# Performance work log

Hardware: AMD Instinct MI355X
Metric: run time of the kernel (lower is better)

The kernel has to match this reference:

```python
import jax, jax.numpy as jnp
import numpy as np

HIDDEN = 1024
N_HEADS = 16
HEAD_DIM = HIDDEN // N_HEADS  # 64


def setup_inputs() -> dict:
    key = jax.random.key(0)
    ks = jax.random.split(key, 5)
    B, S = 4, 4096
    x = jax.random.normal(ks[0], (B, S, HIDDEN), dtype=jnp.float32)
    scale = 1.0 / np.sqrt(HIDDEN)
    wq = jax.random.normal(ks[1], (HIDDEN, HIDDEN), dtype=jnp.float32) * scale
    wk = jax.random.normal(ks[2], (HIDDEN, HIDDEN), dtype=jnp.float32) * scale
    wv = jax.random.normal(ks[3], (HIDDEN, HIDDEN), dtype=jnp.float32) * scale
    wo = jax.random.normal(ks[4], (HIDDEN, HIDDEN), dtype=jnp.float32) * scale
    return {"x": x, "wq": wq, "wk": wk, "wv": wv, "wo": wo}


def reference(x, wq, wk, wv, wo):
    # Weights stored as (out, in) like torch nn.Linear; y = x @ W^T
    B, S, H = x.shape
    q = (x @ wq.T).reshape(B, S, N_HEADS, HEAD_DIM)
    k = (x @ wk.T).reshape(B, S, N_HEADS, HEAD_DIM)
    v = (x @ wv.T).reshape(B, S, N_HEADS, HEAD_DIM)
    # Faithful to original: no transpose to (B,H,S,D) -> scores are over HEADS
    # attn: (B, S, H_heads, H_heads)
    attn = jnp.einsum("bshd,bsgd->bshg", q, k) / np.sqrt(HEAD_DIM)
    attn = jax.nn.softmax(attn, axis=-1)
    out = jnp.einsum("bshg,bsgd->bshd", attn, v).reshape(B, S, H)
    return out @ wo.T
```

## Files before the change

kernel.cpp:

```cpp
#include <hip/hip_runtime.h>
#include <hip/hip_bf16.h>


typedef __bf16 bf16;
typedef __attribute__((ext_vector_type(8))) __bf16 bf16x8;
typedef __attribute__((ext_vector_type(4))) float floatx4;

#define HIDDEN 1024
#define BM 128
#define BN 128
#define BK 32

#define FENCE() asm volatile("" ::: "memory")
#define BAR()                                                                  \
    do {                                                                       \
        FENCE();                                                               \
        __builtin_amdgcn_s_barrier();                                          \
        FENCE();                                                               \
    } while (0)
#define VMCNT(N) asm volatile("s_waitcnt vmcnt(" #N ")" ::: "memory")

__device__ __forceinline__ void async_load16(const bf16* g, bf16* lds) {
    __builtin_amdgcn_global_load_lds(
        (const __attribute__((address_space(1))) void*)g,
        (__attribute__((address_space(3))) void*)lds, 16, 0, 0);
}

__device__ __forceinline__ bf16x8 load8(const bf16* p) {
    return *(const bf16x8*)p;
}
__device__ __forceinline__ bf16x8 load8(const float* p) {
    floatx4 lo = *(const floatx4*)p;
    floatx4 hi = *(const floatx4*)(p + 4);
    bf16x8 r;
#pragma unroll
    for (int i = 0; i < 4; ++i) { r[i] = (bf16)lo[i]; r[i + 4] = (bf16)hi[i]; }
    return r;
}

__global__ __launch_bounds__(256) void cvt_all(
    const float* __restrict__ x,
    const float* __restrict__ wq, const float* __restrict__ wk,
    const float* __restrict__ wv, const float* __restrict__ wo,
    bf16* __restrict__ xb, bf16* __restrict__ wpk, int mh8)
{
    const int per = (HIDDEN * HIDDEN) / 8;
    int i = blockIdx.x * 256 + threadIdx.x;
    if (i < mh8) {
        *(bf16x8*)&xb[(size_t)i * 8] = load8(&x[(size_t)i * 8]);
    } else {
        int j = i - mh8;
        int wsel = j / per;
        int off  = (j - wsel * per) * 8;
        const float* s = wsel == 0 ? wq : wsel == 1 ? wk : wsel == 2 ? wv : wo;
        *(bf16x8*)&wpk[(size_t)j * 8] = load8(&s[off]);
    }
}


template <int S>
__device__ __forceinline__ void stage_half(const bf16* __restrict__ gbase,
                                           int ld, int kt, bf16* lhalf,
                                           int h, int tid) {
#pragma unroll
    for (int j = 0; j < 2; ++j) {
        const int ci = j * 512 + tid;
        const int rr = ci >> 3;
        const int cs = (ci & 7) ^ (rr & 7);
        const int gr = h * S + (rr & (S - 1)) + (rr >> (S == 64 ? 6 : 5)) * (2 * S);
        async_load16(&gbase[(size_t)gr * ld + kt + cs * 8], &lhalf[ci * 8]);
    }
}

__device__ __forceinline__ void ld_a4(const bf16* h, int wm, int col, int quad,
                                      int cx, bf16x8* a) {
#pragma unroll
    for (int i = 0; i < 4; ++i) {
        const int rr = i * 16 + col + (wm << 6);
#pragma unroll
        for (int kk = 0; kk < 2; ++kk)
            a[i * 2 + kk] =
                *(const bf16x8*)&h[rr * 64 + (((kk << 2) + quad) ^ cx) * 8];
    }
}
__device__ __forceinline__ void ld_b2(const bf16* h, int wn, int col, int quad,
                                      int cx, bf16x8* b) {
#pragma unroll
    for (int j = 0; j < 2; ++j) {
        const int rr = j * 16 + col + (wn << 5);
#pragma unroll
        for (int kk = 0; kk < 2; ++kk)
            b[j * 2 + kk] =
                *(const bf16x8*)&h[rr * 64 + (((kk << 2) + quad) ^ cx) * 8];
    }
}

template <int H, int G>
__device__ __forceinline__ void mmq(floatx4 (&acc)[8][4], const bf16x8 (&a)[8],
                                    const bf16x8 (&bb)[4]) {
    __builtin_amdgcn_s_setprio(1);
#pragma unroll
    for (int i = 0; i < 4; ++i)
#pragma unroll
        for (int j = 0; j < 2; ++j)
#pragma unroll
            for (int kk = 0; kk < 2; ++kk)
                acc[H * 4 + i][G * 2 + j] =
                    __builtin_amdgcn_mfma_f32_16x16x32_bf16(
                        a[i * 2 + kk], bb[j * 2 + kk],
                        acc[H * 4 + i][G * 2 + j], 0, 0, 0);
    __builtin_amdgcn_s_setprio(0);
}

template <typename TC>
__global__ __launch_bounds__(512, 2) void gemm8p(
    const bf16* __restrict__ A, const bf16* __restrict__ W,
    TC* __restrict__ C, int K, int lda, int ldc)
{
    __shared__ __align__(16) bf16 sA[2][2][128 * 64];
    __shared__ __align__(16) bf16 sB[2][2][128 * 64];

    const int tid  = threadIdx.x;
    const int lane = tid & 63;
    const int w    = tid >> 6;
    const int wm   = w >> 2;
    const int wn   = w & 3;
    const int m0   = blockIdx.x * 256;
    const int n0   = blockIdx.y * 256;
    const int col  = lane & 15;
    const int quad = lane >> 4;
    const int cx   = col & 7;

    const bf16* Ab = A + (size_t)m0 * lda;
    const bf16* Wb = W + (size_t)n0 * K;

    floatx4 acc[8][4] = {};
    bf16x8 a[8], b0[4], b1[4];

    const int T = K / 64;

    stage_half<64>(Ab, lda, 0, sA[0][0], 0, tid);
    stage_half<32>(Wb, K,   0, sB[0][0], 0, tid);
    stage_half<32>(Wb, K,   0, sB[0][1], 1, tid);
    stage_half<64>(Ab, lda, 0, sA[0][1], 1, tid);
    if (T > 1) {
        stage_half<64>(Ab, lda, 64, sA[1][0], 0, tid);
        stage_half<32>(Wb, K,   64, sB[1][0], 0, tid);
        stage_half<32>(Wb, K,   64, sB[1][1], 1, tid);
        VMCNT(6);
    } else {
        VMCNT(0);
    }
    BAR();

    for (int t = 0; t < T; ++t) {
        const int b   = t & 1;
        const int kt1 = (t + 1) * 64;
        const int kt2 = (t + 2) * 64;

        ld_a4(sA[b][0], wm, col, quad, cx, a);
        ld_b2(sB[b][0], wn, col, quad, cx, b0);
        ld_b2(sB[b][1], wn, col, quad, cx, b1);
        if (t + 1 < T) {
            stage_half<64>(Ab, lda, kt1, sA[b ^ 1][1], 1, tid);
            VMCNT(8);
        } else {
            VMCNT(0);
        }
        BAR();
        mmq<0, 0>(acc, a, b0);
        mmq<0, 1>(acc, a, b1);
        BAR();

        ld_a4(sA[b][1], wm, col, quad, cx, a);
        if (t + 2 < T) {
            stage_half<64>(Ab, lda, kt2, sA[b][0], 0, tid);
            stage_half<32>(Wb, K,   kt2, sB[b][0], 0, tid);
            stage_half<32>(Wb, K,   kt2, sB[b][1], 1, tid);
            VMCNT(8);
        } else {
            VMCNT(0);
        }
        BAR();
        mmq<1, 1>(acc, a, b1);
        mmq<1, 0>(acc, a, b0);
        BAR();
    }

#pragma unroll
    for (int mi = 0; mi < 8; ++mi) {
#pragma unroll
        for (int r = 0; r < 4; ++r) {
            const int row = m0 + wm * 128 + mi * 16 + quad * 4 + r;
#pragma unroll
            for (int ni = 0; ni < 4; ++ni) {
                const int cc = n0 + wn * 64 + ni * 16 + col;
                C[(size_t)row * ldc + cc] = (TC)acc[mi][ni][r];
            }
        }
    }
}

template <typename TA, typename TB, typename TC>
__global__ __launch_bounds__(256, 2) void gemm_bt(
    const TA* __restrict__ A, const TB* __restrict__ W,
    TC* __restrict__ C, int M, int N, int K)
{
    __shared__ __align__(16) bf16 sA[BM * BK];
    __shared__ __align__(16) bf16 sB[BN * BK];

    const int tid  = threadIdx.x;
    const int lane = tid & 63;
    const int w    = tid >> 6;
    const int wm   = w >> 1;
    const int wn   = w & 1;
    const int m0   = blockIdx.x * BM;
    const int n0   = blockIdx.y * BN;
    const int col  = lane & 15;
    const int quad = lane >> 4;

    floatx4 acc[4][4] = {};

    for (int kt = 0; kt < K; kt += BK) {
        bf16x8 ga[2], gb[2];
#pragma unroll
        for (int i = 0; i < 2; ++i) {
            const int c   = i * 256 + tid;
            const int row = c >> 2;
            const int kc  = c & 3;
            ga[i] = load8(&A[(size_t)(m0 + row) * K + kt + kc * 8]);
            gb[i] = load8(&W[(size_t)(n0 + row) * K + kt + kc * 8]);
        }
        __syncthreads();
#pragma unroll
        for (int i = 0; i < 2; ++i) {
            const int c = i * 256 + tid;
            *(bf16x8*)&sA[c * 8] = ga[i];
            *(bf16x8*)&sB[c * 8] = gb[i];
        }
        __syncthreads();

        bf16x8 af[4], bfr[4];
#pragma unroll
        for (int mi = 0; mi < 4; ++mi)
            af[mi] = *(const bf16x8*)&sA[(wm * 64 + mi * 16 + col) * BK + quad * 8];
#pragma unroll
        for (int ni = 0; ni < 4; ++ni)
            bfr[ni] = *(const bf16x8*)&sB[(wn * 64 + ni * 16 + col) * BK + quad * 8];

#pragma unroll
        for (int mi = 0; mi < 4; ++mi)
#pragma unroll
            for (int ni = 0; ni < 4; ++ni)
                acc[mi][ni] = __builtin_amdgcn_mfma_f32_16x16x32_bf16(
                    af[mi], bfr[ni], acc[mi][ni], 0, 0, 0);
    }

#pragma unroll
    for (int mi = 0; mi < 4; ++mi) {
#pragma unroll
        for (int r = 0; r < 4; ++r) {
            const int row = m0 + wm * 64 + mi * 16 + quad * 4 + r;
#pragma unroll
            for (int ni = 0; ni < 4; ++ni) {
                const int cc = n0 + wn * 64 + ni * 16 + col;
                C[(size_t)row * N + cc] = (TC)acc[mi][ni][r];
            }
        }
    }
}

__global__ __launch_bounds__(256) void attn_heads(
    bf16* base, size_t koff, size_t voff, int stride, bf16* ob)
{
    __shared__ __align__(16) bf16 sQ[4][3072];
    __shared__ __align__(16) bf16 sP[4][16 * 40];
    __shared__ __align__(16) bf16 sO[4][1024];

    const int tid   = threadIdx.x;
    const int lane  = tid & 63;
    const int w     = tid >> 6;
    const int token = blockIdx.x * 4 + w;
    const int col   = lane & 15;
    const int quad  = lane >> 4;

    bf16* qt = base + (size_t)token * stride;
    const bf16* src0 = qt;
    const bf16* src1 = qt + koff;
    const bf16* src2 = qt + voff;
    bf16* ot = ob + (size_t)token * HIDDEN;

#pragma unroll
    for (int i = 0; i < 6; ++i) {
        const int ci = i * 64 + lane;
        const int rl = (ci >> 3) & 15;
        const int cs = (ci & 7) ^ (rl & 7);
        const bf16* s = (i < 2) ? src0 : (i < 4) ? src1 : src2;
        async_load16(&s[(rl * 8 + cs) * 8], &sQ[w][ci * 8]);
    }
    VMCNT(0);

    bf16x8 qa[2], kb[2];
#pragma unroll
    for (int kk = 0; kk < 2; ++kk) {
        const int c = ((kk << 2) + quad) ^ (col & 7);
        qa[kk] = *(const bf16x8*)&sQ[w][(col * 8 + c) * 8];
        kb[kk] = *(const bf16x8*)&sQ[w][((16 + col) * 8 + c) * 8];
    }
    floatx4 s = {};
    s = __builtin_amdgcn_mfma_f32_16x16x32_bf16(qa[0], kb[0], s, 0, 0, 0);
    s = __builtin_amdgcn_mfma_f32_16x16x32_bf16(qa[1], kb[1], s, 0, 0, 0);

    bf16x8 va[4] = {};
    if (quad < 2) {
#pragma unroll
        for (int dt = 0; dt < 4; ++dt) {
            const int cb = dt * 2 + (col >> 3);
#pragma unroll
            for (int j = 0; j < 8; ++j) {
                const int r = 32 + quad * 8 + j;
                va[dt][j] = sQ[w][(r * 8 + (cb ^ j)) * 8 + (col & 7)];
            }
        }
    }

#pragma unroll
    for (int r = 0; r < 4; ++r) {
        float e = __expf(s[r] * 0.125f);
        float su = e;
#pragma unroll
        for (int off = 1; off < 16; off <<= 1)
            su += __shfl_xor(su, off);
        sP[w][(quad * 4 + r) * 40 + col] = (bf16)(e / su);
    }

    bf16x8 pa = {};
    if (quad < 2) pa = *(const bf16x8*)&sP[w][col * 40 + quad * 8];
#pragma unroll
    for (int dt = 0; dt < 4; ++dt) {
        floatx4 o4 = {};
        o4 = __builtin_amdgcn_mfma_f32_16x16x32_bf16(va[dt], pa, o4, 0, 0, 0);
        union { bf16 h4[4]; uint2 u; } pk;
#pragma unroll
        for (int r = 0; r < 4; ++r) pk.h4[r] = (bf16)o4[r];
        const int c8 = dt * 4 + quad;
        *(uint2*)&sO[w][(col * 16 + (c8 ^ col)) * 4] = pk.u;
    }

#pragma unroll
    for (int it = 0; it < 4; ++it) {
        const int n8 = it * 64 + lane;
        const int h = n8 >> 4, c8 = n8 & 15;
        const uint2 d = *(const uint2*)&sO[w][(h * 16 + (c8 ^ h)) * 4];
        *(uint2*)&ot[n8 * 4] = d;
    }
}

extern "C" void kernel_launch(void* const* d_in, const int* in_sizes, int n_in,
                              void* d_out, int out_size, void* d_ws, size_t ws_size,
                              hipStream_t stream) {
    const float* x  = (const float*)d_in[0];
    const float* wq = (const float*)d_in[1];
    const float* wk = (const float*)d_in[2];
    const float* wv = (const float*)d_in[3];
    const float* wo = (const float*)d_in[4];
    float* out = (float*)d_out;

    const int M = in_sizes[0] / HIDDEN;
    const size_t MH = (size_t)M * HIDDEN;
    const size_t WH = (size_t)HIDDEN * HIDDEN;

    const size_t need = (MH + 4 * WH + (size_t)M * 3 * HIDDEN) * sizeof(bf16);

    if (ws_size >= need && (M % 256) == 0) {
        bf16* xb  = (bf16*)d_ws;
        bf16* wpk = xb + MH;
        bf16* qkv = wpk + 4 * WH;

        const int mh8 = (int)(MH / 8);
        const int nchunks = mh8 + (int)(4 * WH / 8);
        cvt_all<<<dim3(nchunks / 256), 256, 0, stream>>>(x, wq, wk, wv, wo,
                                                         xb, wpk, mh8);

        gemm8p<bf16><<<dim3(M / 256, 3 * HIDDEN / 256), 512, 0, stream>>>(
            xb, wpk, qkv, HIDDEN, HIDDEN, 3 * HIDDEN);

        attn_heads<<<dim3(M / 4), 256, 0, stream>>>(qkv, 1024, 2048,
                                                    3 * HIDDEN, xb);

        gemm8p<float><<<dim3(M / 256, HIDDEN / 256), 512, 0, stream>>>(
            xb, wpk + 3 * WH, out, HIDDEN, HIDDEN, HIDDEN);
    } else {
        bf16* qb = (bf16*)d_ws;
        bf16* kb = qb + MH;
        bf16* vb = kb + MH;
        dim3 grid(M / BM, HIDDEN / BN), block(256);
        gemm_bt<float, float, bf16><<<grid, block, 0, stream>>>(x, wq, qb, M, HIDDEN, HIDDEN);
        gemm_bt<float, float, bf16><<<grid, block, 0, stream>>>(x, wk, kb, M, HIDDEN, HIDDEN);
        gemm_bt<float, float, bf16><<<grid, block, 0, stream>>>(x, wv, vb, M, HIDDEN, HIDDEN);
        attn_heads<<<dim3(M / 4), block, 0, stream>>>(qb, MH, 2 * MH, HIDDEN, qb);
        gemm_bt<bf16, float, float><<<grid, block, 0, stream>>>(qb, wo, out, M, HIDDEN, HIDDEN);
    }
}
```

Baseline: 291.0 us.

## Double-buffer per-wave token loads in attention kernel, four tokens per wave

Each wave now processes four consecutive tokens and prefetches the next token's Q/K/V into a second LDS buffer while computing the current one, using vmcnt waits tuned to the outstanding loads and stores. The grid shrinks by four. The aim is to hide global load latency in the small per-token head attention. In exchange, LDS per block doubles, which may lower occupancy, and correctness depends on the hand-tuned waitcnt values.

Measured after the change: 292.3 us. No clear change (+0.4%).

```diff
diff --git a/kernel.cpp b/kernel.cpp
--- a/kernel.cpp
+++ b/kernel.cpp
@@ -273,86 +273,95 @@
 __global__ __launch_bounds__(256) void attn_heads(
     bf16* base, size_t koff, size_t voff, int stride, bf16* ob)
 {
-    __shared__ __align__(16) bf16 sQ[4][3072];
+    __shared__ __align__(16) bf16 sQ[4][2][3072];
     __shared__ __align__(16) bf16 sP[4][16 * 40];
     __shared__ __align__(16) bf16 sO[4][1024];
 
     const int tid   = threadIdx.x;
     const int lane  = tid & 63;
     const int w     = tid >> 6;
-    const int token = blockIdx.x * 4 + w;
     const int col   = lane & 15;
     const int quad  = lane >> 4;
-
-    bf16* qt = base + (size_t)token * stride;
-    const bf16* src0 = qt;
-    const bf16* src1 = qt + koff;
-    const bf16* src2 = qt + voff;
-    bf16* ot = ob + (size_t)token * HIDDEN;
-
-#pragma unroll
-    for (int i = 0; i < 6; ++i) {
-        const int ci = i * 64 + lane;
-        const int rl = (ci >> 3) & 15;
-        const int cs = (ci & 7) ^ (rl & 7);
-        const bf16* s = (i < 2) ? src0 : (i < 4) ? src1 : src2;
-        async_load16(&s[(rl * 8 + cs) * 8], &sQ[w][ci * 8]);
-    }
-    VMCNT(0);
-
-    bf16x8 qa[2], kb[2];
-#pragma unroll
-    for (int kk = 0; kk < 2; ++kk) {
-        const int c = ((kk << 2) + quad) ^ (col & 7);
-        qa[kk] = *(const bf16x8*)&sQ[w][(col * 8 + c) * 8];
-        kb[kk] = *(const bf16x8*)&sQ[w][((16 + col) * 8 + c) * 8];
-    }
-    floatx4 s = {};
-    s = __builtin_amdgcn_mfma_f32_16x16x32_bf16(qa[0], kb[0], s, 0, 0, 0);
-    s = __builtin_amdgcn_mfma_f32_16x16x32_bf16(qa[1], kb[1], s, 0, 0, 0);
-
-    bf16x8 va[4] = {};
-    if (quad < 2) {
+    const int t0    = blockIdx.x * 16 + w * 4;
+
+    auto stage = [&](int tok, int s) {
+        const bf16* qt = base + (size_t)tok * stride;
+#pragma unroll
+        for (int i = 0; i < 6; ++i) {
+            const int ci = i * 64 + lane;
+            const int rl = (ci >> 3) & 15;
+            const int cs = (ci & 7) ^ (rl & 7);
+            const bf16* src = (i < 2) ? qt : (i < 4) ? qt + koff : qt + voff;
+            async_load16(&src[(rl * 8 + cs) * 8], &sQ[w][s][ci * 8]);
+        }
+    };
+
+    stage(t0, 0);
+
+#pragma unroll
+    for (int it = 0; it < 4; ++it) {
+        if (it < 3) stage(t0 + it + 1, (it + 1) & 1);
+        if (it == 0)      { VMCNT(6);  }
+        else if (it < 3)  { VMCNT(10); }
+        else              { VMCNT(4);  }
+
+        const bf16* sq = sQ[w][it & 1];
+        bf16* ot = ob + (size_t)(t0 + it) * HIDDEN;
+
+        bf16x8 qa[2], kb[2];
+#pragma unroll
+        for (int kk = 0; kk < 2; ++kk) {
+            const int c = ((kk << 2) + quad) ^ (col & 7);
+            qa[kk] = *(const bf16x8*)&sq[(col * 8 + c) * 8];
+            kb[kk] = *(const bf16x8*)&sq[((16 + col) * 8 + c) * 8];
+        }
+        floatx4 s = {};
+        s = __builtin_amdgcn_mfma_f32_16x16x32_bf16(qa[0], kb[0], s, 0, 0, 0);
+        s = __builtin_amdgcn_mfma_f32_16x16x32_bf16(qa[1], kb[1], s, 0, 0, 0);
+
+        bf16x8 va[4] = {};
+        if (quad < 2) {
+#pragma unroll
+            for (int dt = 0; dt < 4; ++dt) {
+                const int cb = dt * 2 + (col >> 3);
+#pragma unroll
+                for (int j = 0; j < 8; ++j) {
+                    const int r = 32 + quad * 8 + j;
+                    va[dt][j] = sq[(r * 8 + (cb ^ j)) * 8 + (col & 7)];
+                }
+            }
+        }
+
+#pragma unroll
+        for (int r = 0; r < 4; ++r) {
+            float e = __expf(s[r] * 0.125f);
+            float su = e;
+#pragma unroll
+            for (int off = 1; off < 16; off <<= 1)
+                su += __shfl_xor(su, off);
+            sP[w][(quad * 4 + r) * 40 + col] = (bf16)(e / su);
+        }
+
+        bf16x8 pa = {};
+        if (quad < 2) pa = *(const bf16x8*)&sP[w][col * 40 + quad * 8];
 #pragma unroll
         for (int dt = 0; dt < 4; ++dt) {
-            const int cb = dt * 2 + (col >> 3);
-#pragma unroll
-            for (int j = 0; j < 8; ++j) {
-                const int r = 32 + quad * 8 + j;
-                va[dt][j] = sQ[w][(r * 8 + (cb ^ j)) * 8 + (col & 7)];
-            }
-        }
-    }
-
-#pragma unroll
-    for (int r = 0; r < 4; ++r) {
-        float e = __expf(s[r] * 0.125f);
-        float su = e;
-#pragma unroll
-        for (int off = 1; off < 16; off <<= 1)
-            su += __shfl_xor(su, off);
-        sP[w][(quad * 4 + r) * 40 + col] = (bf16)(e / su);
-    }
-
-    bf16x8 pa = {};
-    if (quad < 2) pa = *(const bf16x8*)&sP[w][col * 40 + quad * 8];
-#pragma unroll
-    for (int dt = 0; dt < 4; ++dt) {
-        floatx4 o4 = {};
-        o4 = __builtin_amdgcn_mfma_f32_16x16x32_bf16(va[dt], pa, o4, 0, 0, 0);
-        union { bf16 h4[4]; uint2 u; } pk;
-#pragma unroll
-        for (int r = 0; r < 4; ++r) pk.h4[r] = (bf16)o4[r];
-        const int c8 = dt * 4 + quad;
-        *(uint2*)&sO[w][(col * 16 + (c8 ^ col)) * 4] = pk.u;
-    }
-
-#pragma unroll
-    for (int it = 0; it < 4; ++it) {
-        const int n8 = it * 64 + lane;
-        const int h = n8 >> 4, c8 = n8 & 15;
-        const uint2 d = *(const uint2*)&sO[w][(h * 16 + (c8 ^ h)) * 4];
-        *(uint2*)&ot[n8 * 4] = d;
+            floatx4 o4 = {};
+            o4 = __builtin_amdgcn_mfma_f32_16x16x32_bf16(va[dt], pa, o4, 0, 0, 0);
+            union { bf16 h4[4]; uint2 u; } pk;
+#pragma unroll
+            for (int r = 0; r < 4; ++r) pk.h4[r] = (bf16)o4[r];
+            const int c8 = dt * 4 + quad;
+            *(uint2*)&sO[w][(col * 16 + (c8 ^ col)) * 4] = pk.u;
+        }
+
+#pragma unroll
+        for (int st = 0; st < 4; ++st) {
+            const int n8 = st * 64 + lane;
+            const int h = n8 >> 4, c8 = n8 & 15;
+            const uint2 d = *(const uint2*)&sO[w][(h * 16 + (c8 ^ h)) * 4];
+            *(uint2*)&ot[n8 * 4] = d;
+        }
     }
 }
 
@@ -385,8 +394,8 @@
         gemm8p<bf16><<<dim3(M / 256, 3 * HIDDEN / 256), 512, 0, stream>>>(
             xb, wpk, qkv, HIDDEN, HIDDEN, 3 * HIDDEN);
 
-        attn_heads<<<dim3(M / 4), 256, 0, stream>>>(qkv, 1024, 2048,
-                                                    3 * HIDDEN, xb);
+        attn_heads<<<dim3(M / 16), 256, 0, stream>>>(qkv, 1024, 2048,
+                                                     3 * HIDDEN, xb);
 
         gemm8p<float><<<dim3(M / 256, HIDDEN / 256), 512, 0, stream>>>(
             xb, wpk + 3 * WH, out, HIDDEN, HIDDEN, HIDDEN);
@@ -398,7 +407,7 @@
         gemm_bt<float, float, bf16><<<grid, block, 0, stream>>>(x, wq, qb, M, HIDDEN, HIDDEN);
         gemm_bt<float, float, bf16><<<grid, block, 0, stream>>>(x, wk, kb, M, HIDDEN, HIDDEN);
         gemm_bt<float, float, bf16><<<grid, block, 0, stream>>>(x, wv, vb, M, HIDDEN, HIDDEN);
-        attn_heads<<<dim3(M / 4), block, 0, stream>>>(qb, MH, 2 * MH, HIDDEN, qb);
+        attn_heads<<<dim3(M / 16), block, 0, stream>>>(qb, MH, 2 * MH, HIDDEN, qb);
         gemm_bt<bf16, float, float><<<grid, block, 0, stream>>>(qb, wo, out, M, HIDDEN, HIDDEN);
     }
 }
```
